# Optimization experiments

Hardware: AMD Instinct MI355X
Metric: run time of the kernel (lower is better)

The kernel has to match this reference:

```python
import jax, jax.numpy as jnp
import numpy as np

D_MODEL = 1024
NUM_HEADS = 16
D_FF = 4096
BATCH = 4
SEQ = 1024
EPS = 1e-5
ROPE_THETA = 10000.0


def trunc_normal(key, shape):
    # approximate torch trunc_normal_(mean=0, std=1, a=-2, b=2)
    return jax.random.truncated_normal(key, -2.0, 2.0, shape, dtype=jnp.float32)


def setup_inputs() -> dict:
    key = jax.random.key(0)
    ks = jax.random.split(key, 10)
    d, h, f = D_MODEL, NUM_HEADS, D_FF
    return {
        "x": jax.random.normal(ks[0], (BATCH, SEQ, d), dtype=jnp.float32),
        "wq": trunc_normal(ks[1], (d, d)),
        "wk": trunc_normal(ks[2], (d, d)),
        "wv": trunc_normal(ks[3], (d, d)),
        "wo": trunc_normal(ks[4], (d, d)),
        "w1": trunc_normal(ks[5], (f, d)),
        "w2": trunc_normal(ks[6], (d, f)),
        "w3": trunc_normal(ks[7], (f, d)),
        "g1": trunc_normal(ks[8], (d,)),
        "g2": trunc_normal(ks[9], (d,)),
    }


def rms_norm(x, g):
    # source sums (x^2 + eps) then divides by d -> mean(x^2) + eps
    rms = jnp.sqrt(jnp.mean(jnp.square(x), axis=-1, keepdims=True) + EPS)
    return x * g / rms


def apply_rope(x, pos):
    # x: [b, h, s, d_k]; interleaved-pair rotation, theta=ROPE_THETA
    dk = x.shape[-1]
    inv_freq = ROPE_THETA ** (-jnp.arange(0, dk, 2, dtype=jnp.float32) / dk)
    ang = pos[:, None].astype(jnp.float32) * inv_freq[None, :]  # [s, dk/2]
    cos, sin = jnp.cos(ang), jnp.sin(ang)
    x1, x2 = x[..., 0::2], x[..., 1::2]
    r1 = x1 * cos - x2 * sin
    r2 = x1 * sin + x2 * cos
    return jnp.stack([r1, r2], axis=-1).reshape(x.shape)


def reference(x, wq, wk, wv, wo, w1, w2, w3, g1, g2):
    b, s, d = x.shape
    h, dk = NUM_HEADS, d // NUM_HEADS
    pos = jnp.arange(s)

    # --- attention sub-block (pre-norm) ---
    y = rms_norm(x, g1)
    q = (y @ wq.T).reshape(b, s, h, dk).transpose(0, 2, 1, 3)
    k = (y @ wk.T).reshape(b, s, h, dk).transpose(0, 2, 1, 3)
    v = (y @ wv.T).reshape(b, s, h, dk).transpose(0, 2, 1, 3)
    q = apply_rope(q, pos)
    k = apply_rope(k, pos)
    scores = jnp.einsum('bhqd,bhkd->bhqk', q, k) / jnp.sqrt(jnp.float32(dk))
    causal = jnp.tril(jnp.ones((s, s), dtype=bool))
    scores = jnp.where(causal, scores, -jnp.inf)
    attn = jax.nn.softmax(scores, axis=-1)
    ctx = jnp.einsum('bhqk,bhkd->bhqd', attn, v)
    ctx = ctx.transpose(0, 2, 1, 3).reshape(b, s, d)
    x = x + ctx @ wo.T

    # --- SwiGLU FFN sub-block (pre-norm) ---
    y = rms_norm(x, g2)
    l1 = y @ w1.T
    glu = (jax.nn.sigmoid(l1) * l1) * (y @ w3.T)
    return x + glu @ w2.T
```

## Files before the change

### kernel.cpp

```cpp
#include <hip/hip_runtime.h>

typedef __bf16 bf16;
typedef __attribute__((ext_vector_type(8))) __bf16 bf16x8;
typedef __attribute__((ext_vector_type(4))) float f32x4;

static __device__ __forceinline__ int swz4(int r) { return (r >> 1) & 3; }

static __device__ __forceinline__ void async_cp16(void* lds, const void* g) {
  __builtin_amdgcn_global_load_lds((__attribute__((address_space(1))) void*)g,
                                   (__attribute__((address_space(3))) void*)lds,
                                   16, 0, 0);
}

static __device__ __forceinline__ f32x4 mfma16(bf16x8 a, bf16x8 b, f32x4 c) {
  return __builtin_amdgcn_mfma_f32_16x16x32_bf16(a, b, c, 0, 0, 0);
}

static __device__ __forceinline__ unsigned short bfbits(float f) {
  bf16 b = (bf16)f;
  return __builtin_bit_cast(unsigned short, b);
}

extern "C" __global__ void prep_kernel(
    const float* __restrict__ wq, const float* __restrict__ wk,
    const float* __restrict__ wv, const float* __restrict__ wo,
    const float* __restrict__ w1, const float* __restrict__ w3,
    const float* __restrict__ w2,
    unsigned short* __restrict__ WQH, unsigned short* __restrict__ WQL,
    unsigned short* __restrict__ WKH, unsigned short* __restrict__ WKL,
    unsigned short* __restrict__ WVH, unsigned short* __restrict__ WOH,
    unsigned short* __restrict__ W1H, unsigned short* __restrict__ W3H,
    unsigned short* __restrict__ W2H, float2* __restrict__ rope) {
  const int seg = blockIdx.y;
  const int i = blockIdx.x * 256 + threadIdx.x;
  if (seg == 7) {
    if (i >= 32768) return;
    int s = i >> 5, fi = i & 31;
    float inv_freq = powf(10000.0f, -(2.0f * (float)fi) / 64.0f);
    float ang = (float)s * inv_freq;
    float2 cs;
    cs.x = cosf(ang);
    cs.y = sinf(ang);
    rope[i] = cs;
    return;
  }
  const float* src;
  unsigned short* hi_;
  unsigned short* lo_ = nullptr;
  int n4;
  switch (seg) {
    case 0: src = wq; hi_ = WQH; lo_ = WQL; n4 = 262144; break;
    case 1: src = wk; hi_ = WKH; lo_ = WKL; n4 = 262144; break;
    case 2: src = wv; hi_ = WVH; n4 = 262144; break;
    case 3: src = wo; hi_ = WOH; n4 = 262144; break;
    case 4: src = w1; hi_ = W1H; n4 = 1048576; break;
    case 5: src = w3; hi_ = W3H; n4 = 1048576; break;
    default: src = w2; hi_ = W2H; n4 = 1048576; break;
  }
  if (i >= n4) return;
  float4 v = ((const float4*)src)[i];
  bf16 b0 = (bf16)v.x, b1 = (bf16)v.y, b2 = (bf16)v.z, b3 = (bf16)v.w;
  ushort4 oh;
  oh.x = __builtin_bit_cast(unsigned short, b0);
  oh.y = __builtin_bit_cast(unsigned short, b1);
  oh.z = __builtin_bit_cast(unsigned short, b2);
  oh.w = __builtin_bit_cast(unsigned short, b3);
  ((ushort4*)hi_)[i] = oh;
  if (lo_) {
    ushort4 ol;
    ol.x = bfbits(v.x - (float)b0);
    ol.y = bfbits(v.y - (float)b1);
    ol.z = bfbits(v.z - (float)b2);
    ol.w = bfbits(v.w - (float)b3);
    ((ushort4*)lo_)[i] = ol;
  }
}

extern "C" __global__ __launch_bounds__(256) void rmsnorm_kernel(
    const float* __restrict__ x, const float* __restrict__ g,
    unsigned short* __restrict__ yhi, unsigned short* __restrict__ ylo) {
  int row = blockIdx.x;
  int t = threadIdx.x;
  const float4 xv = *(const float4*)(x + (size_t)row * 1024 + t * 4);
  float ss = xv.x * xv.x + xv.y * xv.y + xv.z * xv.z + xv.w * xv.w;
#pragma unroll
  for (int d = 1; d < 64; d <<= 1) ss += __shfl_xor(ss, d, 64);
  __shared__ float red[4];
  if ((t & 63) == 0) red[t >> 6] = ss;
  __syncthreads();
  float tot = red[0] + red[1] + red[2] + red[3];
  float inv = 1.0f / sqrtf(tot * (1.0f / 1024.0f) + 1e-5f);
  const float4 gv = *(const float4*)(g + t * 4);
  float y0 = xv.x * gv.x * inv, y1 = xv.y * gv.y * inv;
  float y2 = xv.z * gv.z * inv, y3 = xv.w * gv.w * inv;
  bf16 b0 = (bf16)y0, b1 = (bf16)y1, b2 = (bf16)y2, b3 = (bf16)y3;
  ushort4 oh;
  oh.x = __builtin_bit_cast(unsigned short, b0);
  oh.y = __builtin_bit_cast(unsigned short, b1);
  oh.z = __builtin_bit_cast(unsigned short, b2);
  oh.w = __builtin_bit_cast(unsigned short, b3);
  ((ushort4*)yhi)[(size_t)row * 256 + t] = oh;
  if (ylo) {
    ushort4 ol;
    ol.x = bfbits(y0 - (float)b0);
    ol.y = bfbits(y1 - (float)b1);
    ol.z = bfbits(y2 - (float)b2);
    ol.w = bfbits(y3 - (float)b3);
    ((ushort4*)ylo)[(size_t)row * 256 + t] = ol;
  }
}

template <int EPI>
__global__ __launch_bounds__(256, 2) void gemm_nt(
    const bf16* __restrict__ A, const bf16* __restrict__ B, int N, int K, int ldk,
    float* __restrict__ outF, bf16* __restrict__ outB,
    const float* __restrict__ resF) {
  const int bid = blockIdx.x;
  const int xcd = bid & 7, sq = bid >> 3;
  const int z = sq >> 5;
  const int rem = sq & 31;
  const size_t tm = (size_t)(xcd * 4 + (rem >> 3)) * 128;
  const size_t tn = (size_t)(rem & 7) * 128;
  A += (size_t)z * K;
  B += (size_t)z * K;
  __shared__ alignas(16) bf16 As[128 * 64];
  __shared__ alignas(16) bf16 Bs[128 * 64];
  const int tid = threadIdx.x;
  const int lane = tid & 63, wave = tid >> 6;
  const int lo = lane & 15, hi = lane >> 4;
  const int wm = wave >> 1, wn = wave & 1;
  f32x4 acc[4][4] = {};
  for (int k0 = 0; k0 < K; k0 += 64) {
    __syncthreads();
#pragma unroll
    for (int i4 = 0; i4 < 4; i4++) {
      int p = tid + 256 * i4;
      int row = p >> 3, c = p & 7;
      int cs = c ^ (row & 7);
      async_cp16((char*)As + (size_t)p * 16, A + (tm + row) * (size_t)ldk + k0 + cs * 8);
      async_cp16((char*)Bs + (size_t)p * 16, B + (tn + row) * (size_t)ldk + k0 + cs * 8);
    }
    __syncthreads();
#pragma unroll
    for (int kh = 0; kh < 2; kh++) {
      bf16x8 fa[4], fb[4];
#pragma unroll
      for (int i = 0; i < 4; i++) {
        int ra = wm * 64 + i * 16 + lo;
        fa[i] = *(const bf16x8*)((const char*)As + ra * 128 + (((kh * 4 + hi) ^ (ra & 7)) << 4));
        int rb = wn * 64 + i * 16 + lo;
        fb[i] = *(const bf16x8*)((const char*)Bs + rb * 128 + (((kh * 4 + hi) ^ (rb & 7)) << 4));
      }
      __builtin_amdgcn_s_setprio(1);
#pragma unroll
      for (int i = 0; i < 4; i++)
#pragma unroll
        for (int j = 0; j < 4; j++) acc[i][j] = mfma16(fa[i], fb[j], acc[i][j]);
      __builtin_amdgcn_s_setprio(0);
    }
  }
#pragma unroll
  for (int i = 0; i < 4; i++)
#pragma unroll
    for (int j = 0; j < 4; j++)
#pragma unroll
      for (int r = 0; r < 4; r++) {
        size_t m = tm + wm * 64 + i * 16 + hi * 4 + r;
        size_t n = tn + wn * 64 + j * 16 + lo;
        float v = acc[i][j][r];
        if constexpr (EPI == 0) {
          size_t idx = (((m >> 10) * 16 + (n >> 6)) * 64 + (n & 63)) * 1024 + (m & 1023);
          outB[idx] = (bf16)v;
        } else if constexpr (EPI == 1) {
          size_t idx = m * (size_t)N + n;
          outF[idx] = v + resF[idx];
        } else {
          atomicAdd(&outF[m * (size_t)N + n], v);
        }
      }
}

extern "C" __global__ __launch_bounds__(256, 2) void gemm_up_kernel(
    const bf16* __restrict__ A, const bf16* __restrict__ B1,
    const bf16* __restrict__ B3, bf16* __restrict__ G) {
  const int bid = blockIdx.x;
  const int xcd = bid & 7, sq = bid >> 3;
  const size_t tm = (size_t)(xcd * 4 + (sq & 3)) * 128;
  const size_t tn = (size_t)(sq >> 2) * 128;
  __shared__ alignas(16) bf16 As[128 * 64];
  __shared__ alignas(16) bf16 B1s[128 * 64];
  __shared__ alignas(16) bf16 B3s[128 * 64];
  const int tid = threadIdx.x;
  const int lane = tid & 63, wave = tid >> 6;
  const int lo = lane & 15, hi = lane >> 4;
  const int wm = wave >> 1, wn = wave & 1;
  f32x4 acc1[4][4] = {}, acc3[4][4] = {};
  for (int k0 = 0; k0 < 1024; k0 += 64) {
    __syncthreads();
#pragma unroll
    for (int i4 = 0; i4 < 4; i4++) {
      int p = tid + 256 * i4;
      int row = p >> 3, c = p & 7;
      int cs = c ^ (row & 7);
      async_cp16((char*)As + (size_t)p * 16, A + (tm + row) * (size_t)1024 + k0 + cs * 8);
      async_cp16((char*)B1s + (size_t)p * 16, B1 + (tn + row) * (size_t)1024 + k0 + cs * 8);
      async_cp16((char*)B3s + (size_t)p * 16, B3 + (tn + row) * (size_t)1024 + k0 + cs * 8);
    }
    __syncthreads();
#pragma unroll
    for (int kh = 0; kh < 2; kh++) {
      bf16x8 fa[4], fb[4];
#pragma unroll
      for (int i = 0; i < 4; i++) {
        int ra = wm * 64 + i * 16 + lo;
        fa[i] = *(const bf16x8*)((const char*)As + ra * 128 + (((kh * 4 + hi) ^ (ra & 7)) << 4));
        int rb = wn * 64 + i * 16 + lo;
        fb[i] = *(const bf16x8*)((const char*)B1s + rb * 128 + (((kh * 4 + hi) ^ (rb & 7)) << 4));
      }
      __builtin_amdgcn_s_setprio(1);
#pragma unroll
      for (int i = 0; i < 4; i++)
#pragma unroll
        for (int j = 0; j < 4; j++) acc1[i][j] = mfma16(fa[i], fb[j], acc1[i][j]);
      __builtin_amdgcn_s_setprio(0);
#pragma unroll
      for (int j = 0; j < 4; j++) {
        int rb = wn * 64 + j * 16 + lo;
        fb[j] = *(const bf16x8*)((const char*)B3s + rb * 128 + (((kh * 4 + hi) ^ (rb & 7)) << 4));
      }
      __builtin_amdgcn_s_setprio(1);
#pragma unroll
      for (int i = 0; i < 4; i++)
#pragma unroll
        for (int j = 0; j < 4; j++) acc3[i][j] = mfma16(fa[i], fb[j], acc3[i][j]);
      __builtin_amdgcn_s_setprio(0);
    }
  }
#pragma unroll
  for (int i = 0; i < 4; i++)
#pragma unroll
    for (int j = 0; j < 4; j++)
#pragma unroll
      for (int r = 0; r < 4; r++) {
        size_t m = tm + wm * 64 + i * 16 + hi * 4 + r;
        size_t n = tn + wn * 64 + j * 16 + lo;
        float v1 = acc1[i][j][r], v3 = acc3[i][j][r];
        G[m * 4096 + n] = (bf16)(v1 / (1.0f + __expf(-v1)) * v3);
      }
}

extern "C" __global__ __launch_bounds__(256, 2) void gemm_qk_kernel(
    const bf16* __restrict__ Ah, const bf16* __restrict__ Al,
    const bf16* __restrict__ BhQ, const bf16* __restrict__ BlQ,
    const bf16* __restrict__ BhK, const bf16* __restrict__ BlK,
    const float2* __restrict__ rope,
    bf16* __restrict__ OhQ, bf16* __restrict__ OlQ,
    bf16* __restrict__ OhK, bf16* __restrict__ OlK) {
  const int bid = blockIdx.x;
  const int xcd = bid & 7, sq = bid >> 3;
  const int zqk = sq >> 5;
  const int rem = sq & 31;
  const size_t tm = (size_t)(xcd * 4 + (rem >> 3)) * 128;
  const size_t tn = (size_t)(rem & 7) * 128;
  const bf16* Bh = zqk ? BhK : BhQ;
  const bf16* Bl = zqk ? BlK : BlQ;
  bf16* Oh = zqk ? OhK : OhQ;
  bf16* Ol = zqk ? OlK : OlQ;
  __shared__ alignas(16) bf16 Ahs[128 * 64], Als[128 * 64];
  __shared__ alignas(16) bf16 Bhs[128 * 64], Bls[128 * 64];
  const int tid = threadIdx.x;
  const int lane = tid & 63, wave = tid >> 6;
  const int lo = lane & 15, hi = lane >> 4;
  const int wm = wave >> 1, wn = wave & 1;
  const int K = 1024;
  f32x4 acc[4][4] = {};
  for (int k0 = 0; k0 < K; k0 += 64) {
    __syncthreads();
#pragma unroll
    for (int i4 = 0; i4 < 4; i4++) {
      int p = tid + 256 * i4;
      int row = p >> 3, c = p & 7;
      int cs = c ^ (row & 7);
      size_t ga = (tm + row) * (size_t)K + k0 + cs * 8;
      size_t gb = (tn + row) * (size_t)K + k0 + cs * 8;
      async_cp16((char*)Ahs + (size_t)p * 16, Ah + ga);
      async_cp16((char*)Als + (size_t)p * 16, Al + ga);
      async_cp16((char*)Bhs + (size_t)p * 16, Bh + gb);
      async_cp16((char*)Bls + (size_t)p * 16, Bl + gb);
    }
    __syncthreads();
#pragma unroll
    for (int kh = 0; kh < 2; kh++) {
      int offa[4], offb[4];
#pragma unroll
      for (int i = 0; i < 4; i++) {
        int ra = wm * 64 + i * 16 + lo;
        offa[i] = ra * 128 + (((kh * 4 + hi) ^ (ra & 7)) << 4);
        int rb = wn * 64 + i * 16 + lo;
        offb[i] = rb * 128 + (((kh * 4 + hi) ^ (rb & 7)) << 4);
      }
      bf16x8 fah[4], fbh[4], fx[4];
#pragma unroll
      for (int i = 0; i < 4; i++) {
        fah[i] = *(const bf16x8*)((const char*)Ahs + offa[i]);
        fbh[i] = *(const bf16x8*)((const char*)Bhs + offb[i]);
      }
      __builtin_amdgcn_s_setprio(1);
#pragma unroll
      for (int i = 0; i < 4; i++)
#pragma unroll
        for (int j = 0; j < 4; j++) acc[i][j] = mfma16(fah[i], fbh[j], acc[i][j]);
      __builtin_amdgcn_s_setprio(0);
#pragma unroll
      for (int j = 0; j < 4; j++) fx[j] = *(const bf16x8*)((const char*)Bls + offb[j]);
      __builtin_amdgcn_s_setprio(1);
#pragma unroll
      for (int i = 0; i < 4; i++)
#pragma unroll
        for (int j = 0; j < 4; j++) acc[i][j] = mfma16(fah[i], fx[j], acc[i][j]);
      __builtin_amdgcn_s_setprio(0);
#pragma unroll
      for (int i = 0; i < 4; i++) fx[i] = *(const bf16x8*)((const char*)Als + offa[i]);
      __builtin_amdgcn_s_setprio(1);
#pragma unroll
      for (int i = 0; i < 4; i++)
#pragma unroll
        for (int j = 0; j < 4; j++) acc[i][j] = mfma16(fx[i], fbh[j], acc[i][j]);
      __builtin_amdgcn_s_setprio(0);
    }
  }
#pragma unroll
  for (int i = 0; i < 4; i++)
#pragma unroll
    for (int j = 0; j < 4; j++)
#pragma unroll
      for (int r = 0; r < 4; r++) {
        float v = acc[i][j][r];
        float vp = __shfl_xor(v, 1, 64);
        size_t m = tm + wm * 64 + i * 16 + hi * 4 + r;
        size_t n = tn + wn * 64 + j * 16 + lo;
        int s = (int)(m & 1023);
        int pi = (int)((n & 63) >> 1);
        float2 cs = rope[s * 32 + pi];
        float res = (n & 1) ? (vp * cs.y + v * cs.x) : (v * cs.x - vp * cs.y);
        size_t idx = (((m >> 10) * 16 + (n >> 6)) * 1024 + (m & 1023)) * 64 + (n & 63);
        bf16 hb = (bf16)res;
        Oh[idx] = hb;
        Ol[idx] = (bf16)(res - (float)hb);
      }
}

extern "C" __global__ __launch_bounds__(256, 4) void flash_kernel(
    const bf16* __restrict__ qhi, const bf16* __restrict__ qlo,
    const bf16* __restrict__ khi, const bf16* __restrict__ klo,
    const bf16* __restrict__ vT, bf16* __restrict__ ctx) {
  const int bid = blockIdx.x;
  const int qb = bid >> 6;
  const int bh = bid & 63;
  const int tid = threadIdx.x;
  const int wave = tid >> 6, lane = tid & 63;
  const int lo = lane & 15, hi = lane >> 4;

  __shared__ alignas(16) bf16 Ksh[2][64][32];
  __shared__ alignas(16) bf16 Ksl[2][64][32];
  __shared__ alignas(16) bf16 Vs[2][64][32];
  __shared__ alignas(16) bf16 P[4][16][72];

  size_t qoff = ((size_t)bh * 1024 + qb * 64 + wave * 16 + lo) * 64;
  bf16x8 qh[2], ql[2];
#pragma unroll
  for (int ks = 0; ks < 2; ks++) {
    qh[ks] = *(const bf16x8*)(qhi + qoff + ks * 32 + hi * 8);
    ql[ks] = *(const bf16x8*)(qlo + qoff + ks * 32 + hi * 8);
  }

  const int srow = tid >> 2;
  const int scl = (tid & 3) ^ swz4(srow);
  const size_t kgb = (size_t)bh * 1024 * 64;
  const size_t vgb = ((size_t)bh * 64 + srow) * 1024;

  float mrun[4] = {-1e30f, -1e30f, -1e30f, -1e30f};
  float lrun[4] = {0.f, 0.f, 0.f, 0.f};
  f32x4 o[4] = {};
  const float scale = 0.125f;

  for (int kt = 0; kt <= qb; kt++) {
    __syncthreads();
#pragma unroll
    for (int i = 0; i < 2; i++) {
      int p = tid + 256 * i;
      size_t gk = kgb + (size_t)(kt * 64 + srow) * 64 + i * 32 + scl * 8;
      async_cp16((char*)Ksh + (size_t)p * 16, khi + gk);
      async_cp16((char*)Ksl + (size_t)p * 16, klo + gk);
      async_cp16((char*)Vs + (size_t)p * 16, vT + vgb + kt * 64 + i * 32 + scl * 8);
    }
    __syncthreads();

    f32x4 sv[4];
    __builtin_amdgcn_s_setprio(1);
#pragma unroll
    for (int nb = 0; nb < 4; nb++) {
      f32x4 a = {0.f, 0.f, 0.f, 0.f};
#pragma unroll
      for (int ks = 0; ks < 2; ks++) {
        int row = nb * 16 + lo;
        int off16 = (ks * 64 + row) * 4 + (hi ^ swz4(row));
        bf16x8 kh = *(const bf16x8*)((const char*)Ksh + off16 * 16);
        bf16x8 kl = *(const bf16x8*)((const char*)Ksl + off16 * 16);
        a = mfma16(qh[ks], kh, a);
        a = mfma16(qh[ks], kl, a);
        a = mfma16(ql[ks], kh, a);
      }
      sv[nb] = a;
    }
    __builtin_amdgcn_s_setprio(0);

    const bool mt = (kt == qb);
#pragma unroll
    for (int nb = 0; nb < 4; nb++)
#pragma unroll
      for (int r = 0; r < 4; r++) {
        float s = sv[nb][r] * scale;
        if (mt) {
          int kp = nb * 16 + lo;
          int qr = wave * 16 + hi * 4 + r;
          if (kp > qr) s = -1e30f;
        }
        sv[nb][r] = s;
      }
    float mnew[4], rs[4];
#pragma unroll
    for (int r = 0; r < 4; r++) {
      float mx = fmaxf(fmaxf(sv[0][r], sv[1][r]), fmaxf(sv[2][r], sv[3][r]));
#pragma unroll
      for (int d = 1; d < 16; d <<= 1) mx = fmaxf(mx, __shfl_xor(mx, d, 64));
      mnew[r] = fmaxf(mrun[r], mx);
      float sc = __expf(mrun[r] - mnew[r]);
      lrun[r] *= sc;
#pragma unroll
      for (int db = 0; db < 4; db++) o[db][r] *= sc;
      mrun[r] = mnew[r];
      rs[r] = 0.f;
    }
#pragma unroll
    for (int nb = 0; nb < 4; nb++)
#pragma unroll
      for (int r = 0; r < 4; r++) {
        float p = __expf(sv[nb][r] - mnew[r]);
        bf16 pb = (bf16)p;
        rs[r] += (float)pb;
        P[wave][hi * 4 + r][nb * 16 + lo] = pb;
      }
#pragma unroll
    for (int r = 0; r < 4; r++) {
      float t = rs[r];
#pragma unroll
      for (int d = 1; d < 16; d <<= 1) t += __shfl_xor(t, d, 64);
      lrun[r] += t;
    }
    bf16x8 pa[2];
#pragma unroll
    for (int ks = 0; ks < 2; ks++) pa[ks] = *(const bf16x8*)&P[wave][lo][ks * 32 + hi * 8];
    __builtin_amdgcn_s_setprio(1);
#pragma unroll
    for (int db = 0; db < 4; db++)
#pragma unroll
      for (int ks = 0; ks < 2; ks++) {
        int row = db * 16 + lo;
        int off16 = (ks * 64 + row) * 4 + (hi ^ swz4(row));
        bf16x8 vf = *(const bf16x8*)((const char*)Vs + off16 * 16);
        o[db] = mfma16(pa[ks], vf, o[db]);
      }
    __builtin_amdgcn_s_setprio(0);
  }
  int b = bh >> 4, h = bh & 15;
#pragma unroll
  for (int db = 0; db < 4; db++)
#pragma unroll
    for (int r = 0; r < 4; r++) {
      float val = o[db][r] / lrun[r];
      size_t row = (size_t)b * 1024 + qb * 64 + wave * 16 + hi * 4 + r;
      ctx[row * 1024 + h * 64 + db * 16 + lo] = (bf16)val;
    }
}


extern "C" void kernel_launch(void* const* d_in, const int* in_sizes, int n_in,
                              void* d_out, int out_size, void* d_ws, size_t ws_size,
                              hipStream_t stream) {
  (void)in_sizes; (void)n_in; (void)out_size; (void)ws_size;
  const float* x  = (const float*)d_in[0];
  const float* wq = (const float*)d_in[1];
  const float* wk = (const float*)d_in[2];
  const float* wv = (const float*)d_in[3];
  const float* wo = (const float*)d_in[4];
  const float* w1 = (const float*)d_in[5];
  const float* w2 = (const float*)d_in[6];
  const float* w3 = (const float*)d_in[7];
  const float* g1 = (const float*)d_in[8];
  const float* g2 = (const float*)d_in[9];
  float* out = (float*)d_out;

  char* ws = (char*)d_ws;
  size_t off = 0;
  auto alloc = [&](size_t bytes) {
    char* p = ws + off;
    off += (bytes + 255) & ~(size_t)255;
    return p;
  };
  const size_t MB2 = 1024u * 1024u * 2u;
  const size_t MB8 = 4096u * 1024u * 2u;
  void* WQH = alloc(MB2);  void* WQL = alloc(MB2);
  void* WKH = alloc(MB2);  void* WKL = alloc(MB2);
  void* WVH = alloc(MB2);  void* WOH = alloc(MB2);
  void* W1H = alloc(MB8);  void* W3H = alloc(MB8);  void* W2H = alloc(MB8);
  void* ROPE = alloc(32768u * 8u);
  void* Y1H = alloc(MB8);  void* Y1L = alloc(MB8);
  void* QH = alloc(MB8);   void* QL = alloc(MB8);
  void* KH = alloc(MB8);   void* KL = alloc(MB8);
  void* VT = alloc(MB8);
  void* CTX = alloc(MB8);
  void* Y2H = alloc(MB8);
  void* GLU = QH;

  prep_kernel<<<dim3(4096, 8), dim3(256), 0, stream>>>(
      wq, wk, wv, wo, w1, w3, w2,
      (unsigned short*)WQH, (unsigned short*)WQL, (unsigned short*)WKH,
      (unsigned short*)WKL, (unsigned short*)WVH, (unsigned short*)WOH,
      (unsigned short*)W1H, (unsigned short*)W3H, (unsigned short*)W2H,
      (float2*)ROPE);

  rmsnorm_kernel<<<dim3(4096), dim3(256), 0, stream>>>(
      x, g1, (unsigned short*)Y1H, (unsigned short*)Y1L);

  gemm_qk_kernel<<<dim3(512), dim3(256), 0, stream>>>(
      (const bf16*)Y1H, (const bf16*)Y1L,
      (const bf16*)WQH, (const bf16*)WQL, (const bf16*)WKH, (const bf16*)WKL,
      (const float2*)ROPE,
      (bf16*)QH, (bf16*)QL, (bf16*)KH, (bf16*)KL);

  gemm_nt<0><<<dim3(256), dim3(256), 0, stream>>>(
      (const bf16*)Y1H, (const bf16*)WVH, 1024, 1024, 1024,
      nullptr, (bf16*)VT, nullptr);

  flash_kernel<<<dim3(1024), dim3(256), 0, stream>>>(
      (const bf16*)QH, (const bf16*)QL, (const bf16*)KH, (const bf16*)KL,
      (const bf16*)VT, (bf16*)CTX);

  gemm_nt<1><<<dim3(256), dim3(256), 0, stream>>>(
      (const bf16*)CTX, (const bf16*)WOH, 1024, 1024, 1024,
      out, nullptr, x);

  rmsnorm_kernel<<<dim3(4096), dim3(256), 0, stream>>>(
      out, g2, (unsigned short*)Y2H, nullptr);

  gemm_up_kernel<<<dim3(1024), dim3(256), 0, stream>>>(
      (const bf16*)Y2H, (const bf16*)W1H, (const bf16*)W3H, (bf16*)GLU);

  gemm_nt<5><<<dim3(512), dim3(256), 0, stream>>>(
      (const bf16*)GLU, (const bf16*)W2H, 1024, 2048, 4096,
      out, nullptr, nullptr);
}
```

Measured before the change: 290.8 us.

## Double-buffer LDS tiles in GEMM kernels to overlap global loads with MFMA

Converts the gemm_nt, gemm_up and gemm_qk main loops to a two-stage LDS ping-pong. The next K-tile is issued with async global-to-LDS copies while MFMAs run on the current tile, and each iteration ends with a single barrier. For the up and qk kernels the K-tile shrinks from 64 to 32 with a 4-column swizzle, so LDS per block stays the same. The cost is more loop iterations and barriers, and the async copies may not be guaranteed complete before the next-stage reads without an explicit vmcnt wait.

```diff
diff --git a/kernel.cpp b/kernel.cpp
--- a/kernel.cpp
+++ b/kernel.cpp
@@ -123,33 +123,44 @@
   const size_t tn = (size_t)(rem & 7) * 128;
   A += (size_t)z * K;
   B += (size_t)z * K;
-  __shared__ alignas(16) bf16 As[128 * 64];
-  __shared__ alignas(16) bf16 Bs[128 * 64];
+  __shared__ alignas(16) bf16 As[2][128 * 64];
+  __shared__ alignas(16) bf16 Bs[2][128 * 64];
   const int tid = threadIdx.x;
   const int lane = tid & 63, wave = tid >> 6;
   const int lo = lane & 15, hi = lane >> 4;
   const int wm = wave >> 1, wn = wave & 1;
   f32x4 acc[4][4] = {};
-  for (int k0 = 0; k0 < K; k0 += 64) {
-    __syncthreads();
+
+  auto stage = [&](int buf, int k0) {
 #pragma unroll
     for (int i4 = 0; i4 < 4; i4++) {
       int p = tid + 256 * i4;
       int row = p >> 3, c = p & 7;
       int cs = c ^ (row & 7);
-      async_cp16((char*)As + (size_t)p * 16, A + (tm + row) * (size_t)ldk + k0 + cs * 8);
-      async_cp16((char*)Bs + (size_t)p * 16, B + (tn + row) * (size_t)ldk + k0 + cs * 8);
-    }
-    __syncthreads();
+      async_cp16((char*)&As[buf][0] + (size_t)p * 16,
+                 A + (tm + row) * (size_t)ldk + k0 + cs * 8);
+      async_cp16((char*)&Bs[buf][0] + (size_t)p * 16,
+                 B + (tn + row) * (size_t)ldk + k0 + cs * 8);
+    }
+  };
+
+  const int NT = K >> 6;
+  stage(0, 0);
+  __syncthreads();
+  for (int t = 0; t < NT; t++) {
+    const int pb = t & 1;
+    if (t + 1 < NT) stage(pb ^ 1, (t + 1) << 6);
 #pragma unroll
     for (int kh = 0; kh < 2; kh++) {
       bf16x8 fa[4], fb[4];
 #pragma unroll
       for (int i = 0; i < 4; i++) {
         int ra = wm * 64 + i * 16 + lo;
-        fa[i] = *(const bf16x8*)((const char*)As + ra * 128 + (((kh * 4 + hi) ^ (ra & 7)) << 4));
+        fa[i] = *(const bf16x8*)((const char*)&As[pb][0] + ra * 128 +
+                                 (((kh * 4 + hi) ^ (ra & 7)) << 4));
         int rb = wn * 64 + i * 16 + lo;
-        fb[i] = *(const bf16x8*)((const char*)Bs + rb * 128 + (((kh * 4 + hi) ^ (rb & 7)) << 4));
+        fb[i] = *(const bf16x8*)((const char*)&Bs[pb][0] + rb * 128 +
+                                 (((kh * 4 + hi) ^ (rb & 7)) << 4));
       }
       __builtin_amdgcn_s_setprio(1);
 #pragma unroll
@@ -158,6 +169,7 @@
         for (int j = 0; j < 4; j++) acc[i][j] = mfma16(fa[i], fb[j], acc[i][j]);
       __builtin_amdgcn_s_setprio(0);
     }
+    __syncthreads();
   }
 #pragma unroll
   for (int i = 0; i < 4; i++)
@@ -187,54 +199,64 @@
   const int xcd = bid & 7, sq = bid >> 3;
   const size_t tm = (size_t)(xcd * 4 + (sq & 3)) * 128;
   const size_t tn = (size_t)(sq >> 2) * 128;
-  __shared__ alignas(16) bf16 As[128 * 64];
-  __shared__ alignas(16) bf16 B1s[128 * 64];
-  __shared__ alignas(16) bf16 B3s[128 * 64];
+  __shared__ alignas(16) bf16 As[2][128 * 32];
+  __shared__ alignas(16) bf16 B1s[2][128 * 32];
+  __shared__ alignas(16) bf16 B3s[2][128 * 32];
   const int tid = threadIdx.x;
   const int lane = tid & 63, wave = tid >> 6;
   const int lo = lane & 15, hi = lane >> 4;
   const int wm = wave >> 1, wn = wave & 1;
   f32x4 acc1[4][4] = {}, acc3[4][4] = {};
-  for (int k0 = 0; k0 < 1024; k0 += 64) {
+
+  auto stage = [&](int buf, int k0) {
+#pragma unroll
+    for (int i2 = 0; i2 < 2; i2++) {
+      int p = tid + 256 * i2;
+      int r = p >> 2, c = p & 3;
+      int cs = c ^ swz4(r);
+      async_cp16((char*)&As[buf][0] + (size_t)p * 16,
+                 A + (tm + r) * (size_t)1024 + k0 + cs * 8);
+      async_cp16((char*)&B1s[buf][0] + (size_t)p * 16,
+                 B1 + (tn + r) * (size_t)1024 + k0 + cs * 8);
+      async_cp16((char*)&B3s[buf][0] + (size_t)p * 16,
+                 B3 + (tn + r) * (size_t)1024 + k0 + cs * 8);
+    }
+  };
+
+  stage(0, 0);
+  __syncthreads();
+  for (int t = 0; t < 32; t++) {
+    const int pb = t & 1;
+    if (t + 1 < 32) stage(pb ^ 1, (t + 1) << 5);
+    bf16x8 fa[4], fb[4];
+#pragma unroll
+    for (int i = 0; i < 4; i++) {
+      int ra = wm * 64 + i * 16 + lo;
+      fa[i] = *(const bf16x8*)((const char*)&As[pb][0] + ra * 64 +
+                               ((hi ^ swz4(ra)) << 4));
+      int rb = wn * 64 + i * 16 + lo;
+      fb[i] = *(const bf16x8*)((const char*)&B1s[pb][0] + rb * 64 +
+                               ((hi ^ swz4(rb)) << 4));
+    }
+    __builtin_amdgcn_s_setprio(1);
+#pragma unroll
+    for (int i = 0; i < 4; i++)
+#pragma unroll
+      for (int j = 0; j < 4; j++) acc1[i][j] = mfma16(fa[i], fb[j], acc1[i][j]);
+    __builtin_amdgcn_s_setprio(0);
+#pragma unroll
+    for (int j = 0; j < 4; j++) {
+      int rb = wn * 64 + j * 16 + lo;
+      fb[j] = *(const bf16x8*)((const char*)&B3s[pb][0] + rb * 64 +
+                               ((hi ^ swz4(rb)) << 4));
+    }
+    __builtin_amdgcn_s_setprio(1);
+#pragma unroll
+    for (int i = 0; i < 4; i++)
+#pragma unroll
+      for (int j = 0; j < 4; j++) acc3[i][j] = mfma16(fa[i], fb[j], acc3[i][j]);
+    __builtin_amdgcn_s_setprio(0);
     __syncthreads();
-#pragma unroll
-    for (int i4 = 0; i4 < 4; i4++) {
-      int p = tid + 256 * i4;
-      int row = p >> 3, c = p & 7;
-      int cs = c ^ (row & 7);
-      async_cp16((char*)As + (size_t)p * 16, A + (tm + row) * (size_t)1024 + k0 + cs * 8);
-      async_cp16((char*)B1s + (size_t)p * 16, B1 + (tn + row) * (size_t)1024 + k0 + cs * 8);
-      async_cp16((char*)B3s + (size_t)p * 16, B3 + (tn + row) * (size_t)1024 + k0 + cs * 8);
-    }
-    __syncthreads();
-#pragma unroll
-    for (int kh = 0; kh < 2; kh++) {
-      bf16x8 fa[4], fb[4];
-#pragma unroll
-      for (int i = 0; i < 4; i++) {
-        int ra = wm * 64 + i * 16 + lo;
-        fa[i] = *(const bf16x8*)((const char*)As + ra * 128 + (((kh * 4 + hi) ^ (ra & 7)) << 4));
-        int rb = wn * 64 + i * 16 + lo;
-        fb[i] = *(const bf16x8*)((const char*)B1s + rb * 128 + (((kh * 4 + hi) ^ (rb & 7)) << 4));
-      }
-      __builtin_amdgcn_s_setprio(1);
-#pragma unroll
-      for (int i = 0; i < 4; i++)
-#pragma unroll
-        for (int j = 0; j < 4; j++) acc1[i][j] = mfma16(fa[i], fb[j], acc1[i][j]);
-      __builtin_amdgcn_s_setprio(0);
-#pragma unroll
-      for (int j = 0; j < 4; j++) {
-        int rb = wn * 64 + j * 16 + lo;
-        fb[j] = *(const bf16x8*)((const char*)B3s + rb * 128 + (((kh * 4 + hi) ^ (rb & 7)) << 4));
-      }
-      __builtin_amdgcn_s_setprio(1);
-#pragma unroll
-      for (int i = 0; i < 4; i++)
-#pragma unroll
-        for (int j = 0; j < 4; j++) acc3[i][j] = mfma16(fa[i], fb[j], acc3[i][j]);
-      __builtin_amdgcn_s_setprio(0);
-    }
   }
 #pragma unroll
   for (int i = 0; i < 4; i++)
@@ -266,68 +288,73 @@
   const bf16* Bl = zqk ? BlK : BlQ;
   bf16* Oh = zqk ? OhK : OhQ;
   bf16* Ol = zqk ? OlK : OlQ;
-  __shared__ alignas(16) bf16 Ahs[128 * 64], Als[128 * 64];
-  __shared__ alignas(16) bf16 Bhs[128 * 64], Bls[128 * 64];
+  __shared__ alignas(16) bf16 Ahs[2][128 * 32], Als[2][128 * 32];
+  __shared__ alignas(16) bf16 Bhs[2][128 * 32], Bls[2][128 * 32];
   const int tid = threadIdx.x;
   const int lane = tid & 63, wave = tid >> 6;
   const int lo = lane & 15, hi = lane >> 4;
   const int wm = wave >> 1, wn = wave & 1;
-  const int K = 1024;
   f32x4 acc[4][4] = {};
-  for (int k0 = 0; k0 < K; k0 += 64) {
+
+  auto stage = [&](int buf, int k0) {
+#pragma unroll
+    for (int i2 = 0; i2 < 2; i2++) {
+      int p = tid + 256 * i2;
+      int r = p >> 2, c = p & 3;
+      int cs = c ^ swz4(r);
+      size_t ga = (tm + r) * (size_t)1024 + k0 + cs * 8;
+      size_t gb = (tn + r) * (size_t)1024 + k0 + cs * 8;
+      async_cp16((char*)&Ahs[buf][0] + (size_t)p * 16, Ah + ga);
+      async_cp16((char*)&Als[buf][0] + (size_t)p * 16, Al + ga);
+      async_cp16((char*)&Bhs[buf][0] + (size_t)p * 16, Bh + gb);
+      async_cp16((char*)&Bls[buf][0] + (size_t)p * 16, Bl + gb);
+    }
+  };
+
+  stage(0, 0);
+  __syncthreads();
+  for (int t = 0; t < 32; t++) {
+    const int pb = t & 1;
+    if (t + 1 < 32) stage(pb ^ 1, (t + 1) << 5);
+    int offa[4], offb[4];
+#pragma unroll
+    for (int i = 0; i < 4; i++) {
+      int ra = wm * 64 + i * 16 + lo;
+      offa[i] = ra * 64 + ((hi ^ swz4(ra)) << 4);
+      int rb = wn * 64 + i * 16 + lo;
+      offb[i] = rb * 64 + ((hi ^ swz4(rb)) << 4);
+    }
+    bf16x8 fah[4], fbh[4], fx[4];
+#pragma unroll
+    for (int i = 0; i < 4; i++) {
+      fah[i] = *(const bf16x8*)((const char*)&Ahs[pb][0] + offa[i]);
+      fbh[i] = *(const bf16x8*)((const char*)&Bhs[pb][0] + offb[i]);
+    }
+    __builtin_amdgcn_s_setprio(1);
+#pragma unroll
+    for (int i = 0; i < 4; i++)
+#pragma unroll
+      for (int j = 0; j < 4; j++) acc[i][j] = mfma16(fah[i], fbh[j], acc[i][j]);
+    __builtin_amdgcn_s_setprio(0);
+#pragma unroll
+    for (int j = 0; j < 4; j++)
+      fx[j] = *(const bf16x8*)((const char*)&Bls[pb][0] + offb[j]);
+    __builtin_amdgcn_s_setprio(1);
+#pragma unroll
+    for (int i = 0; i < 4; i++)
+#pragma unroll
+      for (int j = 0; j < 4; j++) acc[i][j] = mfma16(fah[i], fx[j], acc[i][j]);
+    __builtin_amdgcn_s_setprio(0);
+#pragma unroll
+    for (int i = 0; i < 4; i++)
+      fx[i] = *(const bf16x8*)((const char*)&Als[pb][0] + offa[i]);
+    __builtin_amdgcn_s_setprio(1);
+#pragma unroll
+    for (int i = 0; i < 4; i++)
+#pragma unroll
+      for (int j = 0; j < 4; j++) acc[i][j] = mfma16(fx[i], fbh[j], acc[i][j]);
+    __builtin_amdgcn_s_setprio(0);
     __syncthreads();
-#pragma unroll
-    for (int i4 = 0; i4 < 4; i4++) {
-      int p = tid + 256 * i4;
-      int row = p >> 3, c = p & 7;
-      int cs = c ^ (row & 7);
-      size_t ga = (tm + row) * (size_t)K + k0 + cs * 8;
-      size_t gb = (tn + row) * (size_t)K + k0 + cs * 8;
-      async_cp16((char*)Ahs + (size_t)p * 16, Ah + ga);
-      async_cp16((char*)Als + (size_t)p * 16, Al + ga);
-      async_cp16((char*)Bhs + (size_t)p * 16, Bh + gb);
-      async_cp16((char*)Bls + (size_t)p * 16, Bl + gb);
-    }
-    __syncthreads();
-#pragma unroll
-    for (int kh = 0; kh < 2; kh++) {
-      int offa[4], offb[4];
-#pragma unroll
-      for (int i = 0; i < 4; i++) {
-        int ra = wm * 64 + i * 16 + lo;
-        offa[i] = ra * 128 + (((kh * 4 + hi) ^ (ra & 7)) << 4);
-        int rb = wn * 64 + i * 16 + lo;
-        offb[i] = rb * 128 + (((kh * 4 + hi) ^ (rb & 7)) << 4);
-      }
-      bf16x8 fah[4], fbh[4], fx[4];
-#pragma unroll
-      for (int i = 0; i < 4; i++) {
-        fah[i] = *(const bf16x8*)((const char*)Ahs + offa[i]);
-        fbh[i] = *(const bf16x8*)((const char*)Bhs + offb[i]);
-      }
-      __builtin_amdgcn_s_setprio(1);
-#pragma unroll
-      for (int i = 0; i < 4; i++)
-#pragma unroll
-        for (int j = 0; j < 4; j++) acc[i][j] = mfma16(fah[i], fbh[j], acc[i][j]);
-      __builtin_amdgcn_s_setprio(0);
-#pragma unroll
-      for (int j = 0; j < 4; j++) fx[j] = *(const bf16x8*)((const char*)Bls + offb[j]);
-      __builtin_amdgcn_s_setprio(1);
-#pragma unroll
-      for (int i = 0; i < 4; i++)
-#pragma unroll
-        for (int j = 0; j < 4; j++) acc[i][j] = mfma16(fah[i], fx[j], acc[i][j]);
-      __builtin_amdgcn_s_setprio(0);
-#pragma unroll
-      for (int i = 0; i < 4; i++) fx[i] = *(const bf16x8*)((const char*)Als + offa[i]);
-      __builtin_amdgcn_s_setprio(1);
-#pragma unroll
-      for (int i = 0; i < 4; i++)
-#pragma unroll
-        for (int j = 0; j < 4; j++) acc[i][j] = mfma16(fx[i], fbh[j], acc[i][j]);
-      __builtin_amdgcn_s_setprio(0);
-    }
   }
 #pragma unroll
   for (int i = 0; i < 4; i++)
```

Measured after the change: 304.6 us. 1.05x slower.
